# Kernel tuning notes

Measured on AMD Instinct MI355X. Metric: run time of the kernel, lower is better.

## Reference

```python
import jax, jax.numpy as jnp
import numpy as np
import math

EMBED = 1024
HEADS = 16
HEAD_DIM = EMBED // HEADS


def setup_inputs() -> dict:
    key = jax.random.key(0)
    ks = jax.random.split(key, 6)
    scale = 1.0 / math.sqrt(EMBED)
    x = jax.random.normal(ks[0], (4, 2048, EMBED), dtype=jnp.float32)
    Wv = jax.random.normal(ks[1], (EMBED, EMBED), dtype=jnp.float32) * scale
    Wk = jax.random.normal(ks[2], (EMBED, EMBED), dtype=jnp.float32) * scale
    Wq = jax.random.normal(ks[3], (EMBED, EMBED), dtype=jnp.float32) * scale
    Wo = jax.random.normal(ks[4], (EMBED, EMBED), dtype=jnp.float32) * scale
    bo = jax.random.normal(ks[5], (EMBED,), dtype=jnp.float32) * 0.02
    return {"x": x, "Wq": Wq, "Wk": Wk, "Wv": Wv, "Wo": Wo, "bo": bo}


def reference(x, Wq, Wk, Wv, Wo, bo):
    N, S, E = x.shape
    H, D = HEADS, HEAD_DIM
    # Linear(E,E,bias=False): y = x @ W.T ; weights here stored as [out,in]
    q = (x @ Wq.T).reshape(N, S, H, D)
    k = (x @ Wk.T).reshape(N, S, H, D)
    v = (x @ Wv.T).reshape(N, S, H, D)
    energy = jnp.einsum('nqhd,nkhd->nhqk', q, k)  # [N,H,S,S]
    attn = jax.nn.softmax(energy / math.sqrt(D), axis=-1)
    out = jnp.einsum('nhql,nlhd->nqhd', attn, v).reshape(N, S, E)
    return out @ Wo.T + bo
```

## Files before the change

kernel.cpp:

```cpp
#include <hip/hip_runtime.h>
#include <stdint.h>

#define NB   4
#define SLEN 2048
#define EMB  1024
#define NH   16
#define HD   64
#define MTOT (NB * SLEN)

typedef __bf16 bf8_t  __attribute__((ext_vector_type(8)));
typedef __bf16 bf4_t  __attribute__((ext_vector_type(4)));
typedef float  f4_t   __attribute__((ext_vector_type(4)));

#if __has_builtin(__builtin_amdgcn_exp2f)
#define EXP2(x) __builtin_amdgcn_exp2f(x)
#else
#define EXP2(x) exp2f(x)
#endif

__device__ __forceinline__ void gld16(const void* g, void* l) {
    __builtin_amdgcn_global_load_lds(
        (__attribute__((address_space(1))) void*)(g),
        (__attribute__((address_space(3))) void*)(l),
        16, 0, 0);
}

__device__ __forceinline__ uint32_t pack_bf16_rtn(float a, float b) {
    uint32_t ua = __builtin_bit_cast(uint32_t, a) + 0x8000u;
    uint32_t ub = __builtin_bit_cast(uint32_t, b) + 0x8000u;
    return __builtin_amdgcn_perm(ub, ua, 0x07060302u);
}
__device__ __forceinline__ uint32_t pack_bf16_rtz(float a, float b) {
    return __builtin_amdgcn_perm(__builtin_bit_cast(uint32_t, b),
                                 __builtin_bit_cast(uint32_t, a), 0x07060302u);
}

__global__ __launch_bounds__(256) void cast_all(const float* __restrict__ x,
                                                const float* __restrict__ Wq,
                                                const float* __restrict__ Wk,
                                                const float* __restrict__ Wv,
                                                const float* __restrict__ Wo,
                                                __bf16* __restrict__ xb,
                                                __bf16* __restrict__ wb) {
    int b = blockIdx.x;
    const float* s;
    __bf16* d;
    if (b < 8192) {
        s = x; d = xb;
    } else {
        int y = (b - 8192) >> 10;
        s = (y == 0) ? Wq : (y == 1) ? Wk : (y == 2) ? Wv : Wo;
        d = wb + (size_t)y * (EMB * EMB);
        b = (b - 8192) & 1023;
    }
    int i = (b * 256 + (int)threadIdx.x) * 4;
    float4 f = *(const float4*)(s + i);
    bf4_t o = { (__bf16)f.x, (__bf16)f.y, (__bf16)f.z, (__bf16)f.w };
    *(bf4_t*)(d + i) = o;
}

template <int MODE>
__global__ __launch_bounds__(256) void gemm_bt(const __bf16* __restrict__ A,
                                               const __bf16* __restrict__ B,
                                               void* __restrict__ Cv,
                                               const float* __restrict__ bias,
                                               int M, int N, int K) {
    __shared__ __bf16 As[128 * 64];
    __shared__ __bf16 Bs[128 * 64];

    const int tid  = threadIdx.x;
    const int lane = tid & 63;
    const int w    = tid >> 6;
    const int quad = lane >> 4;
    const int l16  = lane & 15;
    const int m0   = blockIdx.x * 128;
    const int n0   = blockIdx.y * 128;
    const int wm   = (w >> 1) * 64;
    const int wn   = (w & 1) * 64;

    f4_t acc[4][4];
#pragma unroll
    for (int i = 0; i < 4; ++i)
#pragma unroll
        for (int j = 0; j < 4; ++j) acc[i][j] = (f4_t){0.f, 0.f, 0.f, 0.f};

    for (int k0 = 0; k0 < K; k0 += 64) {
        __syncthreads();
#pragma unroll
        for (int t = 0; t < 4; ++t) {
            int c   = t * 256 + tid;
            int row = c >> 3;
            int kc  = (c & 7) ^ (row & 7);
            int cb  = c & ~63;
            gld16(A + (size_t)(m0 + row) * K + k0 + kc * 8, &As[cb * 8]);
            gld16(B + (size_t)(n0 + row) * K + k0 + kc * 8, &Bs[cb * 8]);
        }
        __syncthreads();
#pragma unroll
        for (int ks = 0; ks < 2; ++ks) {
            bf8_t af[4], bfr[4];
#pragma unroll
            for (int i = 0; i < 4; ++i) {
                int r = wm + i * 16 + l16;
                af[i] = *(const bf8_t*)&As[r * 64 + (((ks * 4 + quad) ^ (r & 7)) * 8)];
            }
#pragma unroll
            for (int j = 0; j < 4; ++j) {
                int r = wn + j * 16 + l16;
                bfr[j] = *(const bf8_t*)&Bs[r * 64 + (((ks * 4 + quad) ^ (r & 7)) * 8)];
            }
#pragma unroll
            for (int i = 0; i < 4; ++i)
#pragma unroll
                for (int j = 0; j < 4; ++j) {
                    if (MODE == 1)
                        acc[i][j] = __builtin_amdgcn_mfma_f32_16x16x32_bf16(
                            af[i], bfr[j], acc[i][j], 0, 0, 0);
                    else
                        acc[i][j] = __builtin_amdgcn_mfma_f32_16x16x32_bf16(
                            bfr[j], af[i], acc[i][j], 0, 0, 0);
                }
        }
    }

#pragma unroll
    for (int i = 0; i < 4; ++i) {
#pragma unroll
        for (int j = 0; j < 4; ++j) {
            if (MODE == 0) {
                int m   = m0 + wm + i * 16 + l16;
                int col = n0 + wn + j * 16 + quad * 4;
                __bf16* qb = (__bf16*)Cv;
                __bf16* dst = (col < 1024) ? qb : qb + (size_t)8 * 1024 * 1024;
                bf4_t pk = { (__bf16)acc[i][j][0], (__bf16)acc[i][j][1],
                             (__bf16)acc[i][j][2], (__bf16)acc[i][j][3] };
                *(bf4_t*)&dst[(size_t)m * 1024 + (col & 1023)] = pk;
            } else if (MODE == 1) {
                int m   = m0 + wm + i * 16 + quad * 4;
                int col = n0 + wn + j * 16 + l16;
                __bf16* vtb = (__bf16*)Cv;
                size_t idx = ((size_t)(m >> 11) * 1024 + col) * 2048 + (m & 2047);
                bf4_t pk = { (__bf16)acc[i][j][0], (__bf16)acc[i][j][1],
                             (__bf16)acc[i][j][2], (__bf16)acc[i][j][3] };
                *(bf4_t*)&vtb[idx] = pk;
            } else {
                int m   = m0 + wm + i * 16 + l16;
                int col = n0 + wn + j * 16 + quad * 4;
                float* Cf = (float*)Cv;
                float4 bv = *(const float4*)&bias[col];
                float4 ov = { acc[i][j][0] + bv.x, acc[i][j][1] + bv.y,
                              acc[i][j][2] + bv.z, acc[i][j][3] + bv.w };
                *(float4*)&Cf[(size_t)m * N + col] = ov;
            }
        }
    }
}

__device__ __forceinline__ void attn_stage(const __bf16* __restrict__ kbase,
                                           const __bf16* __restrict__ vbase,
                                           int l0, int tid,
                                           __bf16* __restrict__ Ksb,
                                           __bf16* __restrict__ Vsb) {
#pragma unroll
    for (int t = 0; t < 2; ++t) {
        int c   = t * 256 + tid;
        int row = c >> 3;
        int kc  = (c & 7) ^ (row & 7);
        int cb  = c & ~63;
        gld16(kbase + (size_t)(l0 + row) * EMB + kc * 8, Ksb + cb * 8);
        gld16(vbase + (size_t)row * SLEN + l0 + kc * 8, Vsb + cb * 8);
    }
}

__device__ __forceinline__ void attn_tile(const __bf16* __restrict__ Ksb,
                                          const __bf16* __restrict__ Vsb,
                                          __bf16* __restrict__ pw,
                                          const bf8_t (*bq)[2], bf8_t aones,
                                          f4_t* ls, f4_t (*o)[4],
                                          int quad, int l16, int sw) {
#pragma unroll
    for (int jk = 0; jk < 4; ++jk) {
        bf8_t ak[2];
#pragma unroll
        for (int ks = 0; ks < 2; ++ks)
            ak[ks] = *(const bf8_t*)&Ksb[(jk * 16 + l16) * 64 +
                                         (((ks * 4 + quad) ^ sw) * 8)];
#pragma unroll
        for (int jq = 0; jq < 4; ++jq) {
            f4_t e = (f4_t){0.f, 0.f, 0.f, 0.f};
            e = __builtin_amdgcn_mfma_f32_16x16x32_bf16(ak[0], bq[jq][0], e, 0, 0, 0);
            e = __builtin_amdgcn_mfma_f32_16x16x32_bf16(ak[1], bq[jq][1], e, 0, 0, 0);
            uint32_t d0 = pack_bf16_rtz(EXP2(e[0]), EXP2(e[1]));
            uint32_t d1 = pack_bf16_rtz(EXP2(e[2]), EXP2(e[3]));
            *(uint2*)&pw[(jq * 16 + l16) * 72 + jk * 16 + quad * 4] = (uint2){d0, d1};
        }
    }
#pragma unroll
    for (int ks = 0; ks < 2; ++ks) {
        bf8_t bp[4];
#pragma unroll
        for (int jq = 0; jq < 4; ++jq)
            bp[jq] = *(const bf8_t*)&pw[(jq * 16 + l16) * 72 + ks * 32 + quad * 8];
#pragma unroll
        for (int jq = 0; jq < 4; ++jq)
            ls[jq] = __builtin_amdgcn_mfma_f32_16x16x32_bf16(aones, bp[jq], ls[jq], 0, 0, 0);
#pragma unroll
        for (int jd = 0; jd < 4; ++jd) {
            bf8_t av = *(const bf8_t*)&Vsb[(jd * 16 + l16) * 64 +
                                           (((ks * 4 + quad) ^ sw) * 8)];
#pragma unroll
            for (int jq = 0; jq < 4; ++jq)
                o[jq][jd] = __builtin_amdgcn_mfma_f32_16x16x32_bf16(av, bp[jq],
                                                                    o[jq][jd], 0, 0, 0);
        }
    }
}

__global__ __launch_bounds__(256, 2) void attn_fwd(const __bf16* __restrict__ Q,
                                                   const __bf16* __restrict__ K,
                                                   const __bf16* __restrict__ Vt,
                                                   __bf16* __restrict__ O) {
    __shared__ __bf16 Ks0[64 * 64];
    __shared__ __bf16 Ks1[64 * 64];
    __shared__ __bf16 Vs0[64 * 64];
    __shared__ __bf16 Vs1[64 * 64];
    __shared__ __bf16 Ps[4 * 64 * 72];

    const int tid  = threadIdx.x;
    const int lane = tid & 63;
    const int w    = tid >> 6;
    const int quad = lane >> 4;
    const int l16  = lane & 15;
    const int nh   = blockIdx.y;
    const int n    = nh >> 4;
    const int h    = nh & 15;
    const int q0   = blockIdx.x * 256 + w * 64;

    const float QSCALE = 0.125f * 1.44269504f;

    bf8_t bq[4][2];
#pragma unroll
    for (int jq = 0; jq < 4; ++jq)
#pragma unroll
        for (int ks = 0; ks < 2; ++ks) {
            bf8_t v = *(const bf8_t*)(Q + (size_t)(n * SLEN + q0 + jq * 16 + l16) * EMB +
                                      h * HD + ks * 32 + quad * 8);
#pragma unroll
            for (int t = 0; t < 8; ++t) v[t] = (__bf16)((float)v[t] * QSCALE);
            bq[jq][ks] = v;
        }

    bf8_t aones;
#pragma unroll
    for (int t = 0; t < 8; ++t) aones[t] = (__bf16)1.0f;

    f4_t ls[4];
    f4_t o[4][4];
#pragma unroll
    for (int jq = 0; jq < 4; ++jq) {
        ls[jq] = (f4_t){0.f, 0.f, 0.f, 0.f};
#pragma unroll
        for (int jd = 0; jd < 4; ++jd) o[jq][jd] = (f4_t){0.f, 0.f, 0.f, 0.f};
    }

    const __bf16* kbase = K + (size_t)n * SLEN * EMB + h * HD;
    const __bf16* vbase = Vt + (size_t)nh * HD * SLEN;
    __bf16* pw = Ps + w * 64 * 72;
    const int sw = l16 & 7;

    attn_stage(kbase, vbase, 0, tid, Ks0, Vs0);

    for (int it = 0; it < 32; it += 2) {
        int l0 = it * 64;
        __syncthreads();
        attn_stage(kbase, vbase, l0 + 64, tid, Ks1, Vs1);
        attn_tile(Ks0, Vs0, pw, bq, aones, ls, o, quad, l16, sw);
        __syncthreads();
        int lnn = (l0 + 128 < SLEN) ? l0 + 128 : l0 + 64;
        attn_stage(kbase, vbase, lnn, tid, Ks0, Vs0);
        attn_tile(Ks1, Vs1, pw, bq, aones, ls, o, quad, l16, sw);
    }

#pragma unroll
    for (int jq = 0; jq < 4; ++jq) {
        float inv = 1.0f / ls[jq][0];
#pragma unroll
        for (int jd = 0; jd < 4; ++jd) {
            uint32_t d0 = pack_bf16_rtn(o[jq][jd][0] * inv, o[jq][jd][1] * inv);
            uint32_t d1 = pack_bf16_rtn(o[jq][jd][2] * inv, o[jq][jd][3] * inv);
            *(uint2*)&O[(size_t)(n * SLEN + q0 + jq * 16 + l16) * EMB + h * HD +
                        jd * 16 + quad * 4] = (uint2){d0, d1};
        }
    }
}

extern "C" void kernel_launch(void* const* d_in, const int* in_sizes, int n_in,
                              void* d_out, int out_size, void* d_ws, size_t ws_size,
                              hipStream_t stream) {
    const float* x  = (const float*)d_in[0];
    const float* Wq = (const float*)d_in[1];
    const float* Wk = (const float*)d_in[2];
    const float* Wv = (const float*)d_in[3];
    const float* Wo = (const float*)d_in[4];
    const float* bo = (const float*)d_in[5];

    char* wsb = (char*)d_ws;
    const size_t MB = (size_t)1 << 20;
    __bf16* xb  = (__bf16*)(wsb + 0 * MB);
    __bf16* ab  = xb;
    __bf16* wqb = (__bf16*)(wsb + 16 * MB);
    __bf16* wvb = (__bf16*)(wsb + 20 * MB);
    __bf16* wob = (__bf16*)(wsb + 22 * MB);
    __bf16* qb  = (__bf16*)(wsb + 24 * MB);
    __bf16* kb  = (__bf16*)(wsb + 40 * MB);
    __bf16* vtb = (__bf16*)(wsb + 56 * MB);

    cast_all<<<dim3(12288), dim3(256), 0, stream>>>(x, Wq, Wk, Wv, Wo, xb, wqb);

    gemm_bt<0><<<dim3(MTOT / 128, 2048 / 128), 256, 0, stream>>>(
        xb, wqb, qb, nullptr, MTOT, 1024, EMB);

    gemm_bt<1><<<dim3(MTOT / 128, 1024 / 128), 256, 0, stream>>>(
        xb, wvb, vtb, nullptr, MTOT, 1024, EMB);

    attn_fwd<<<dim3(SLEN / 256, NB * NH), 256, 0, stream>>>(qb, kb, vtb, ab);

    gemm_bt<2><<<dim3(MTOT / 128, EMB / 128), 256, 0, stream>>>(
        ab, wob, d_out, bo, MTOT, EMB, EMB);
}
```

Baseline: 265.5 us.

## Double-buffer GEMM LDS staging and fuse Q/K/V projections into one launch

```diff
diff --git a/kernel.cpp b/kernel.cpp
--- a/kernel.cpp
+++ b/kernel.cpp
@@ -59,14 +59,79 @@
     *(bf4_t*)(d + i) = o;
 }
 
-template <int MODE>
-__global__ __launch_bounds__(256) void gemm_bt(const __bf16* __restrict__ A,
-                                               const __bf16* __restrict__ B,
-                                               void* __restrict__ Cv,
-                                               const float* __restrict__ bias,
-                                               int M, int N, int K) {
-    __shared__ __bf16 As[128 * 64];
-    __shared__ __bf16 Bs[128 * 64];
+__device__ __forceinline__ void gstage(const __bf16* __restrict__ A,
+                                       const __bf16* __restrict__ B,
+                                       int m0, int n0, int k0, int K, int tid,
+                                       __bf16* __restrict__ As,
+                                       __bf16* __restrict__ Bs) {
+#pragma unroll
+    for (int t = 0; t < 4; ++t) {
+        int c   = t * 256 + tid;
+        int row = c >> 3;
+        int kc  = (c & 7) ^ (row & 7);
+        int cb  = c & ~63;
+        gld16(A + (size_t)(m0 + row) * K + k0 + kc * 8, As + cb * 8);
+        gld16(B + (size_t)(n0 + row) * K + k0 + kc * 8, Bs + cb * 8);
+    }
+}
+
+template <bool SWAP>
+__device__ __forceinline__ void gcompute(const __bf16* __restrict__ As,
+                                         const __bf16* __restrict__ Bs,
+                                         f4_t (*acc)[4],
+                                         int wm, int wn, int quad, int l16) {
+#pragma unroll
+    for (int ks = 0; ks < 2; ++ks) {
+        bf8_t af[4], bfr[4];
+#pragma unroll
+        for (int i = 0; i < 4; ++i) {
+            int r = wm + i * 16 + l16;
+            af[i] = *(const bf8_t*)&As[r * 64 + (((ks * 4 + quad) ^ (r & 7)) * 8)];
+        }
+#pragma unroll
+        for (int j = 0; j < 4; ++j) {
+            int r = wn + j * 16 + l16;
+            bfr[j] = *(const bf8_t*)&Bs[r * 64 + (((ks * 4 + quad) ^ (r & 7)) * 8)];
+        }
+#pragma unroll
+        for (int i = 0; i < 4; ++i)
+#pragma unroll
+            for (int j = 0; j < 4; ++j) {
+                if (SWAP)
+                    acc[i][j] = __builtin_amdgcn_mfma_f32_16x16x32_bf16(
+                        bfr[j], af[i], acc[i][j], 0, 0, 0);
+                else
+                    acc[i][j] = __builtin_amdgcn_mfma_f32_16x16x32_bf16(
+                        af[i], bfr[j], acc[i][j], 0, 0, 0);
+            }
+    }
+}
+
+template <bool SWAP>
+__device__ __forceinline__ void gkloop(const __bf16* __restrict__ A,
+                                       const __bf16* __restrict__ B,
+                                       int m0, int n0, int K, int tid,
+                                       __bf16* As0, __bf16* Bs0,
+                                       __bf16* As1, __bf16* Bs1,
+                                       f4_t (*acc)[4],
+                                       int wm, int wn, int quad, int l16) {
+    gstage(A, B, m0, n0, 0, K, tid, As0, Bs0);
+    for (int k0 = 0; k0 < K; k0 += 128) {
+        __syncthreads();
+        gstage(A, B, m0, n0, k0 + 64, K, tid, As1, Bs1);
+        gcompute<SWAP>(As0, Bs0, acc, wm, wn, quad, l16);
+        __syncthreads();
+        int knn = (k0 + 128 < K) ? k0 + 128 : k0 + 64;
+        gstage(A, B, m0, n0, knn, K, tid, As0, Bs0);
+        gcompute<SWAP>(As1, Bs1, acc, wm, wn, quad, l16);
+    }
+}
+
+__global__ __launch_bounds__(256, 2) void proj_qkv(const __bf16* __restrict__ A,
+                                                   const __bf16* __restrict__ B,
+                                                   __bf16* __restrict__ qb) {
+    __shared__ __bf16 As0[128 * 64], Bs0[128 * 64];
+    __shared__ __bf16 As1[128 * 64], Bs1[128 * 64];
 
     const int tid  = threadIdx.x;
     const int lane = tid & 63;
@@ -84,76 +149,72 @@
 #pragma unroll
         for (int j = 0; j < 4; ++j) acc[i][j] = (f4_t){0.f, 0.f, 0.f, 0.f};
 
-    for (int k0 = 0; k0 < K; k0 += 64) {
-        __syncthreads();
-#pragma unroll
-        for (int t = 0; t < 4; ++t) {
-            int c   = t * 256 + tid;
-            int row = c >> 3;
-            int kc  = (c & 7) ^ (row & 7);
-            int cb  = c & ~63;
-            gld16(A + (size_t)(m0 + row) * K + k0 + kc * 8, &As[cb * 8]);
-            gld16(B + (size_t)(n0 + row) * K + k0 + kc * 8, &Bs[cb * 8]);
-        }
-        __syncthreads();
-#pragma unroll
-        for (int ks = 0; ks < 2; ++ks) {
-            bf8_t af[4], bfr[4];
-#pragma unroll
-            for (int i = 0; i < 4; ++i) {
-                int r = wm + i * 16 + l16;
-                af[i] = *(const bf8_t*)&As[r * 64 + (((ks * 4 + quad) ^ (r & 7)) * 8)];
-            }
+    if (n0 < 2048) {
+        gkloop<true>(A, B, m0, n0, EMB, tid, As0, Bs0, As1, Bs1, acc, wm, wn, quad, l16);
+#pragma unroll
+        for (int i = 0; i < 4; ++i)
 #pragma unroll
             for (int j = 0; j < 4; ++j) {
-                int r = wn + j * 16 + l16;
-                bfr[j] = *(const bf8_t*)&Bs[r * 64 + (((ks * 4 + quad) ^ (r & 7)) * 8)];
-            }
-#pragma unroll
-            for (int i = 0; i < 4; ++i)
-#pragma unroll
-                for (int j = 0; j < 4; ++j) {
-                    if (MODE == 1)
-                        acc[i][j] = __builtin_amdgcn_mfma_f32_16x16x32_bf16(
-                            af[i], bfr[j], acc[i][j], 0, 0, 0);
-                    else
-                        acc[i][j] = __builtin_amdgcn_mfma_f32_16x16x32_bf16(
-                            bfr[j], af[i], acc[i][j], 0, 0, 0);
-                }
-        }
-    }
-
-#pragma unroll
-    for (int i = 0; i < 4; ++i) {
-#pragma unroll
-        for (int j = 0; j < 4; ++j) {
-            if (MODE == 0) {
                 int m   = m0 + wm + i * 16 + l16;
                 int col = n0 + wn + j * 16 + quad * 4;
-                __bf16* qb = (__bf16*)Cv;
                 __bf16* dst = (col < 1024) ? qb : qb + (size_t)8 * 1024 * 1024;
                 bf4_t pk = { (__bf16)acc[i][j][0], (__bf16)acc[i][j][1],
                              (__bf16)acc[i][j][2], (__bf16)acc[i][j][3] };
                 *(bf4_t*)&dst[(size_t)m * 1024 + (col & 1023)] = pk;
-            } else if (MODE == 1) {
-                int m   = m0 + wm + i * 16 + quad * 4;
-                int col = n0 + wn + j * 16 + l16;
-                __bf16* vtb = (__bf16*)Cv;
-                size_t idx = ((size_t)(m >> 11) * 1024 + col) * 2048 + (m & 2047);
+            }
+    } else {
+        gkloop<false>(A, B, m0, n0, EMB, tid, As0, Bs0, As1, Bs1, acc, wm, wn, quad, l16);
+        __bf16* vtb = qb + (size_t)16 * 1024 * 1024;
+#pragma unroll
+        for (int i = 0; i < 4; ++i)
+#pragma unroll
+            for (int j = 0; j < 4; ++j) {
+                int m  = m0 + wm + i * 16 + quad * 4;
+                int ch = n0 - 2048 + wn + j * 16 + l16;
+                size_t idx = ((size_t)(m >> 11) * 1024 + ch) * 2048 + (m & 2047);
                 bf4_t pk = { (__bf16)acc[i][j][0], (__bf16)acc[i][j][1],
                              (__bf16)acc[i][j][2], (__bf16)acc[i][j][3] };
                 *(bf4_t*)&vtb[idx] = pk;
-            } else {
-                int m   = m0 + wm + i * 16 + l16;
-                int col = n0 + wn + j * 16 + quad * 4;
-                float* Cf = (float*)Cv;
-                float4 bv = *(const float4*)&bias[col];
-                float4 ov = { acc[i][j][0] + bv.x, acc[i][j][1] + bv.y,
-                              acc[i][j][2] + bv.z, acc[i][j][3] + bv.w };
-                *(float4*)&Cf[(size_t)m * N + col] = ov;
             }
-        }
-    }
+    }
+}
+
+__global__ __launch_bounds__(256, 2) void gemm_out(const __bf16* __restrict__ A,
+                                                   const __bf16* __restrict__ B,
+                                                   float* __restrict__ C,
+                                                   const float* __restrict__ bias) {
+    __shared__ __bf16 As0[128 * 64], Bs0[128 * 64];
+    __shared__ __bf16 As1[128 * 64], Bs1[128 * 64];
+
+    const int tid  = threadIdx.x;
+    const int lane = tid & 63;
+    const int w    = tid >> 6;
+    const int quad = lane >> 4;
+    const int l16  = lane & 15;
+    const int m0   = blockIdx.x * 128;
+    const int n0   = blockIdx.y * 128;
+    const int wm   = (w >> 1) * 64;
+    const int wn   = (w & 1) * 64;
+
+    f4_t acc[4][4];
+#pragma unroll
+    for (int i = 0; i < 4; ++i)
+#pragma unroll
+        for (int j = 0; j < 4; ++j) acc[i][j] = (f4_t){0.f, 0.f, 0.f, 0.f};
+
+    gkloop<true>(A, B, m0, n0, EMB, tid, As0, Bs0, As1, Bs1, acc, wm, wn, quad, l16);
+
+#pragma unroll
+    for (int i = 0; i < 4; ++i)
+#pragma unroll
+        for (int j = 0; j < 4; ++j) {
+            int m   = m0 + wm + i * 16 + l16;
+            int col = n0 + wn + j * 16 + quad * 4;
+            float4 bv = *(const float4*)&bias[col];
+            float4 ov = { acc[i][j][0] + bv.x, acc[i][j][1] + bv.y,
+                          acc[i][j][2] + bv.z, acc[i][j][3] + bv.w };
+            *(float4*)&C[(size_t)m * EMB + col] = ov;
+        }
 }
 
 __device__ __forceinline__ void attn_stage(const __bf16* __restrict__ kbase,
@@ -309,7 +370,6 @@
     __bf16* xb  = (__bf16*)(wsb + 0 * MB);
     __bf16* ab  = xb;
     __bf16* wqb = (__bf16*)(wsb + 16 * MB);
-    __bf16* wvb = (__bf16*)(wsb + 20 * MB);
     __bf16* wob = (__bf16*)(wsb + 22 * MB);
     __bf16* qb  = (__bf16*)(wsb + 24 * MB);
     __bf16* kb  = (__bf16*)(wsb + 40 * MB);
@@ -317,14 +377,9 @@
 
     cast_all<<<dim3(12288), dim3(256), 0, stream>>>(x, Wq, Wk, Wv, Wo, xb, wqb);
 
-    gemm_bt<0><<<dim3(MTOT / 128, 2048 / 128), 256, 0, stream>>>(
-        xb, wqb, qb, nullptr, MTOT, 1024, EMB);
-
-    gemm_bt<1><<<dim3(MTOT / 128, 1024 / 128), 256, 0, stream>>>(
-        xb, wvb, vtb, nullptr, MTOT, 1024, EMB);
+    proj_qkv<<<dim3(MTOT / 128, 3072 / 128), 256, 0, stream>>>(xb, wqb, qb);
 
     attn_fwd<<<dim3(SLEN / 256, NB * NH), 256, 0, stream>>>(qb, kb, vtb, ab);
 
-    gemm_bt<2><<<dim3(MTOT / 128, EMB / 128), 256, 0, stream>>>(
-        ab, wob, d_out, bo, MTOT, EMB, EMB);
-}
+    gemm_out<<<dim3(MTOT / 128, EMB / 128), 256, 0, stream>>>(ab, wob, (float*)d_out, bo);
+}
```

After: 248.9 us. -6.2%, faster.
